# Kernel optimization log

Hardware: AMD Instinct MI355X
Metric: run time of the kernel (lower is better)

## Reference

```python
import jax, jax.numpy as jnp
import numpy as np

B, H, W, T, D = 8, 32, 32, 4, 768
BLK = 4  # super-block of base tokens used to generate the static partition


def _build_descs():
    """Deterministic partition: 4x4 blocks of the 32x32 grid, scale = block_idx % 3."""
    d0, d1, d2 = [], [], []
    for t in range(T):
        i = 0
        for by in range(0, H, BLK):
            for bx in range(0, W, BLK):
                s = i % 3
                i += 1
                if s == 0:  # 16 base (scale-0) tokens
                    for yy in range(by, by + BLK):
                        for xx in range(bx, bx + BLK):
                            d0.append((yy, xx, t))
                elif s == 1:  # four 2x2 (scale-1) tokens
                    for yy in range(by, by + BLK, 2):
                        for xx in range(bx, bx + BLK, 2):
                            d1.append((yy, xx, t))
                else:  # one 4x4 (scale-2) token
                    d2.append((by, bx, t))
    return (jnp.asarray(np.array(d0, dtype=np.int32)),
            jnp.asarray(np.array(d1, dtype=np.int32)),
            jnp.asarray(np.array(d2, dtype=np.int32)))


def setup_inputs() -> dict:
    key = jax.random.key(0)
    ks = jax.random.split(key, 8)
    base = jax.random.normal(ks[0], (B, H, W, T, D), dtype=jnp.float32)
    desc0, desc1, desc2 = _build_descs()  # [1408,3], [336,3], [84,3] of (y, x, t)
    ws = 0.05  # keep conv outputs O(1)
    w1 = jax.random.normal(ks[1], (D, D, 2, 2), jnp.float32) * ws
    b1 = jax.random.normal(ks[2], (D,), jnp.float32) * ws
    w2a = jax.random.normal(ks[3], (D, D, 2, 2), jnp.float32) * ws
    b2a = jax.random.normal(ks[4], (D,), jnp.float32) * ws
    w2b = jax.random.normal(ks[5], (D, D, 2, 2), jnp.float32) * ws
    b2b = jax.random.normal(ks[6], (D,), jnp.float32) * ws
    return {"base_patch_embeddings": base, "desc0": desc0, "desc1": desc1,
            "desc2": desc2, "w1": w1, "b1": b1, "w2a": w2a, "b2a": b2a,
            "w2b": w2b, "b2b": b2b}


def _gather_blocks(base, desc, S):
    """Gather [B, N, S, S, D] blocks at (y, x, t) descriptors."""
    off = jnp.arange(S)
    ys = desc[:, 0][:, None, None] + off[None, :, None]  # [N,S,1]
    xs = desc[:, 1][:, None, None] + off[None, None, :]  # [N,1,S]
    ts = desc[:, 2][:, None, None]                       # [N,1,1]
    return base[:, ys, xs, ts, :]                        # [B,N,S,S,D]


def _down(x, w, b):
    """One k=2, s=2 conv over grouped blocks: [B,N,S,S,D] -> [B,N,S/2,S/2,D]."""
    Bn, N, S, _, Dd = x.shape
    x = x.reshape(Bn, N, S // 2, 2, S // 2, 2, Dd)
    return jnp.einsum('bnhiwjc,dcij->bnhwd', x, w) + b


def reference(base_patch_embeddings, desc0, desc1, desc2, w1, b1, w2a, b2a, w2b, b2b):
    base = base_patch_embeddings
    # scale 0: direct gather of base tokens
    tok0 = base[:, desc0[:, 0], desc0[:, 1], desc0[:, 2], :]          # [B,N0,D]
    # scale 1: 2x2 blocks -> one conv
    blk1 = _gather_blocks(base, desc1, 2)                             # [B,N1,2,2,D]
    tok1 = _down(blk1, w1, b1)[:, :, 0, 0, :]                         # [B,N1,D]
    # scale 2: 4x4 blocks -> two convs
    blk2 = _gather_blocks(base, desc2, 4)                             # [B,N2,4,4,D]
    tok2 = _down(_down(blk2, w2a, b2a), w2b, b2b)[:, :, 0, 0, :]      # [B,N2,D]
    tokens = jnp.concatenate([tok0, tok1, tok2], axis=1)              # [B,1828,D]
    # positions: (y, x, size_in_base, timestep)
    def _pos(desc, size):
        n = desc.shape[0]
        return jnp.concatenate([desc[:, :2],
                                jnp.full((n, 1), size, jnp.int32),
                                desc[:, 2:3]], axis=1)
    positions = jnp.concatenate([_pos(desc0, 1), _pos(desc1, 2), _pos(desc2, 4)], axis=0)
    return tokens, positions
```

## Files before the change

### kernel.cpp

```cpp
#include <hip/hip_runtime.h>
#include <cstdint>
#include <cstddef>

#define BB    8
#define HH    32
#define WW    32
#define TT    4
#define DD    768
#define N0    1408
#define N1    336
#define N2    84
#define NTOK  1828
#define TOK_FLOATS (BB*NTOK*DD)
#define KDIM  3072
#define M1    (BB*N1)
#define M2A   (BB*N2*4)
#define M2B   (BB*N2)

typedef __attribute__((ext_vector_type(8))) short          short8v;
typedef __attribute__((ext_vector_type(8))) unsigned short us8;
typedef __attribute__((ext_vector_type(4))) float          f32x4;

__device__ __forceinline__ unsigned short f2bf(float f) {
    unsigned int u = __float_as_uint(f);
    u += 0x7fffu + ((u >> 16) & 1u);
    return (unsigned short)(u >> 16);
}

__device__ __forceinline__ void cp16(const unsigned short* g, unsigned short* l) {
    __builtin_amdgcn_global_load_lds(
        (const __attribute__((address_space(1))) unsigned int*)(const void*)g,
        (__attribute__((address_space(3))) unsigned int*)(void*)l,
        16, 0, 0);
}

#define GA_BLKS 8064
#define CW_BLKS 6912
#define G0_BLKS 2048
#define PREP_BLKS (GA_BLKS + CW_BLKS + G0_BLKS + 8)

__global__ __launch_bounds__(256) void prep_kernel(
    const float* __restrict__ base, const int* __restrict__ d0,
    const int* __restrict__ d1, const int* __restrict__ d2,
    const float* __restrict__ w1, const float* __restrict__ w2a,
    const float* __restrict__ w2b,
    unsigned short* __restrict__ A1, unsigned short* __restrict__ A2,
    unsigned short* __restrict__ W1, unsigned short* __restrict__ W2a,
    unsigned short* __restrict__ W2b,
    float* __restrict__ out, float* __restrict__ pos)
{
    const int blk = blockIdx.x, tid = threadIdx.x;
    if (blk < GA_BLKS) {
        int idx = blk * 256 + tid;
        int rm = idx / 384, o = idx - rm * 384;
        int s = (o & ~7) | ((o ^ rm) & 7);
        int p = s / 96, c0 = (s - p * 96) * 8;
        const float* rowp;
        unsigned short* dst;
        if (rm < M1) {
            int m = rm, b = m / N1, tok = m - b * N1;
            int y = d1[tok*3] + (p>>1), x = d1[tok*3+1] + (p&1), t = d1[tok*3+2];
            rowp = base + (size_t)(((b*HH + y)*WW + x)*TT + t) * DD;
            dst  = A1 + (size_t)m * KDIM + o * 8;
        } else {
            int m = rm - M1, b = m / (N2*4), r = m - b * (N2*4);
            int n = r >> 2, hw = r & 3, h = hw >> 1, w = hw & 1;
            int y = d2[n*3] + 2*h + (p>>1), x = d2[n*3+1] + 2*w + (p&1), t = d2[n*3+2];
            rowp = base + (size_t)(((b*HH + y)*WW + x)*TT + t) * DD;
            dst  = A2 + (size_t)m * KDIM + o * 8;
        }
        float4 v0 = *(const float4*)(rowp + c0);
        float4 v1 = *(const float4*)(rowp + c0 + 4);
        us8 r8;
        r8[0]=f2bf(v0.x); r8[1]=f2bf(v0.y); r8[2]=f2bf(v0.z); r8[3]=f2bf(v0.w);
        r8[4]=f2bf(v1.x); r8[5]=f2bf(v1.y); r8[6]=f2bf(v1.z); r8[7]=f2bf(v1.w);
        *(us8*)dst = r8;
    } else if (blk < GA_BLKS + CW_BLKS) {
        int r = blk - GA_BLKS;
        int wsel = r / 2304;
        int idx  = (r - wsel * 2304) * 256 + tid;
        const float* w        = wsel==0 ? w1 : (wsel==1 ? w2a : w2b);
        unsigned short* Wt    = wsel==0 ? W1 : (wsel==1 ? W2a : W2b);
        int d = idx / DD, c = idx - d * DD;
        float4 v = *(const float4*)(w + (size_t)d * KDIM + c * 4);
        int csw = (c & ~63) | ((((c>>3) ^ d) & 7) << 3) | (c & 7);
        unsigned short* o = Wt + (size_t)d * KDIM + csw;
        o[0*DD] = f2bf(v.x); o[1*DD] = f2bf(v.y); o[2*DD] = f2bf(v.z); o[3*DD] = f2bf(v.w);
    } else if (blk < GA_BLKS + CW_BLKS + G0_BLKS) {
        int bl = blk - GA_BLKS - CW_BLKS;
        const int total = BB * N0 * (DD/4);
        for (int idx = bl * 256 + tid; idx < total; idx += G0_BLKS * 256) {
            int d4 = idx % (DD/4);
            int nb = idx / (DD/4);
            int n  = nb % N0;
            int b  = nb / N0;
            int y = d0[n*3], x = d0[n*3+1], t = d0[n*3+2];
            const float4* src = (const float4*)(base + (size_t)(((b*HH + y)*WW + x)*TT + t) * DD) + d4;
            float4*       dst = (float4*)(out + ((size_t)b*NTOK + n) * DD) + d4;
            *dst = *src;
        }
    } else {
        int n = (blk - GA_BLKS - CW_BLKS - G0_BLKS) * 256 + tid;
        if (n >= NTOK) return;
        int y, x, t, s;
        if (n < N0)         { y = d0[n*3];         x = d0[n*3+1];         t = d0[n*3+2];       s = 1; }
        else if (n < N0+N1) { int m = n - N0;      y = d1[m*3]; x = d1[m*3+1]; t = d1[m*3+2];  s = 2; }
        else                { int m = n - N0 - N1; y = d2[m*3]; x = d2[m*3+1]; t = d2[m*3+2];  s = 4; }
        pos[n*4+0] = (float)y; pos[n*4+1] = (float)x; pos[n*4+2] = (float)s; pos[n*4+3] = (float)t;
    }
}

struct GCfg {
    const unsigned short* A;
    const unsigned short* Bw;
    const float*          bias;
    float*                outf;
    unsigned short*       outb;
    int                   M;
    int                   mode;
};

__global__ __launch_bounds__(256) void mfma_gemm_v3(
    GCfg c0, GCfg c1, int nper, int mblks, int swz)
{
    __shared__ unsigned short As[2][64 * 64];
    __shared__ unsigned short Bs[2][128 * 64];

    int wgid = blockIdx.x;
    if (swz) wgid = (wgid & 7) * (gridDim.x >> 3) + (wgid >> 3);
    GCfg cfg = c0;
    if (wgid >= nper) { cfg = c1; wgid -= nper; }
    const int nb = wgid / mblks, mb = wgid - nb * mblks;
    const int m0 = mb * 64, n0 = nb * 128;

    const int tid = threadIdx.x, lane = tid & 63;
    const int wv = tid >> 6, wr = wv >> 1, wc = wv & 1;
    const int lr = lane & 15, lq = lane >> 4, xr = lr & 7;

    const int aoct = tid & 7, trow = tid >> 3;
    int am0 = m0 + trow;      if (am0 >= cfg.M) am0 = cfg.M - 1;
    int am1 = m0 + 32 + trow; if (am1 >= cfg.M) am1 = cfg.M - 1;
    const unsigned short* ag0 = cfg.A + (size_t)am0 * KDIM + aoct * 8;
    const unsigned short* ag1 = cfg.A + (size_t)am1 * KDIM + aoct * 8;
    const unsigned short* bg0 = cfg.Bw + (size_t)(n0 +      trow) * KDIM + aoct * 8;
    const unsigned short* bg1 = cfg.Bw + (size_t)(n0 + 32 + trow) * KDIM + aoct * 8;
    const unsigned short* bg2 = cfg.Bw + (size_t)(n0 + 64 + trow) * KDIM + aoct * 8;
    const unsigned short* bg3 = cfg.Bw + (size_t)(n0 + 96 + trow) * KDIM + aoct * 8;

    const int wu = tid & 192;

    f32x4 acc[2][4];
    #pragma unroll
    for (int i = 0; i < 2; ++i)
        #pragma unroll
        for (int j = 0; j < 4; ++j)
            #pragma unroll
            for (int r = 0; r < 4; ++r) acc[i][j][r] = 0.f;

    auto STAGE = [&](int buf, int k0) {
        cp16(ag0 + k0, &As[buf][(0*256 + wu) * 8]);
        cp16(ag1 + k0, &As[buf][(1*256 + wu) * 8]);
        cp16(bg0 + k0, &Bs[buf][(0*256 + wu) * 8]);
        cp16(bg1 + k0, &Bs[buf][(1*256 + wu) * 8]);
        cp16(bg2 + k0, &Bs[buf][(2*256 + wu) * 8]);
        cp16(bg3 + k0, &Bs[buf][(3*256 + wu) * 8]);
    };

    STAGE(0, 0);
    constexpr int NIT = KDIM / 64;
    for (int it = 0; it < NIT; ++it) {
        const int cur = it & 1;
        if (it + 1 < NIT) {
            STAGE(cur ^ 1, (it + 1) * 64);
            asm volatile("s_waitcnt vmcnt(6)" ::: "memory");
        } else {
            asm volatile("s_waitcnt vmcnt(0)" ::: "memory");
        }
        __builtin_amdgcn_s_barrier();
        const unsigned short* Asb = As[cur];
        const unsigned short* Bsb = Bs[cur];
        #pragma unroll
        for (int ks = 0; ks < 2; ++ks) {
            short8v av[2], bv[4];
            #pragma unroll
            for (int fm = 0; fm < 2; ++fm) {
                int row = wr*32 + fm*16 + lr;
                av[fm] = *(const short8v*)&Asb[row*64 + ((ks*4 + lq) ^ xr) * 8];
            }
            #pragma unroll
            for (int fn = 0; fn < 4; ++fn) {
                int row = wc*64 + fn*16 + lr;
                bv[fn] = *(const short8v*)&Bsb[row*64 + ((ks*4 + lq) ^ xr) * 8];
            }
            #pragma unroll
            for (int fm = 0; fm < 2; ++fm)
                #pragma unroll
                for (int fn = 0; fn < 4; ++fn)
                    acc[fm][fn] = __builtin_amdgcn_mfma_f32_16x16x32_bf16(
                        av[fm], bv[fn], acc[fm][fn], 0, 0, 0);
        }
        __builtin_amdgcn_s_barrier();
    }

    const int mode = cfg.mode;
    #pragma unroll
    for (int fm = 0; fm < 2; ++fm) {
        #pragma unroll
        for (int fn = 0; fn < 4; ++fn) {
            int n = n0 + wc*64 + fn*16 + lr;
            float bs = cfg.bias[n];
            #pragma unroll
            for (int r = 0; r < 4; ++r) {
                int m = m0 + wr*32 + fm*16 + lq*4 + r;
                if (m >= cfg.M) continue;
                float v = acc[fm][fn][r] + bs;
                if (mode == 0) {
                    int b = m / N1, tok = m - b*N1;
                    cfg.outf[((size_t)b*NTOK + N0 + tok)*DD + n] = v;
                } else if (mode == 1) {
                    int nsw = (n & ~63) | ((((n>>3) ^ (m>>2)) & 7) << 3) | (n & 7);
                    cfg.outb[(size_t)m*DD + nsw] = f2bf(v);
                } else {
                    int b = m / N2, tk = m - b*N2;
                    cfg.outf[((size_t)b*NTOK + N0 + N1 + tk)*DD + n] = v;
                }
            }
        }
    }
}

extern "C" void kernel_launch(void* const* d_in, const int* in_sizes, int n_in,
                              void* d_out, int out_size, void* d_ws, size_t ws_size,
                              hipStream_t stream)
{
    const float* base  = (const float*)d_in[0];
    const int*   desc0 = (const int*)  d_in[1];
    const int*   desc1 = (const int*)  d_in[2];
    const int*   desc2 = (const int*)  d_in[3];
    const float* w1    = (const float*)d_in[4];
    const float* b1    = (const float*)d_in[5];
    const float* w2a   = (const float*)d_in[6];
    const float* b2a   = (const float*)d_in[7];
    const float* w2b   = (const float*)d_in[8];
    const float* b2b   = (const float*)d_in[9];

    float* out = (float*)d_out;
    float* pos = (float*)d_out + TOK_FLOATS;
    unsigned short* ws = (unsigned short*)d_ws;

    const size_t ABF = (size_t)M1 * KDIM;
    const size_t Y1  = (size_t)M2A * DD;
    const size_t WTB = (size_t)DD * KDIM;
    unsigned short* A1  = ws;
    unsigned short* A2  = A1  + ABF;
    unsigned short* y1b = A2  + ABF;
    unsigned short* W1  = y1b + Y1;
    unsigned short* W2a = W1  + WTB;
    unsigned short* W2b = W2a + WTB;

    prep_kernel<<<PREP_BLKS, 256, 0, stream>>>(
        base, desc0, desc1, desc2, w1, w2a, w2b,
        A1, A2, W1, W2a, W2b, out, pos);

    GCfg cA = { A1, W1,  b1,  out,     nullptr, M1,  0 };
    GCfg cB = { A2, W2a, b2a, nullptr, y1b,     M2A, 1 };
    mfma_gemm_v3<<<504, 256, 0, stream>>>(cA, cB, 252, 42, 1);

    GCfg cC = { y1b, W2b, b2b, out, nullptr, M2B, 2 };
    mfma_gemm_v3<<<66, 256, 0, stream>>>(cC, cC, 66, 11, 0);
}
```

Before: 296.4 us.

## Use 128x128 tiles with 32x32 MFMA, split-K final GEMM, and overlap gather copy

The GEMM tile grows from 64x128 to 128x128 and switches to the 32x32x16 bf16 MFMA, and workgroups are remapped per XCD. The last small GEMM is split along K into two halves that accumulate into a pre-zeroed output with atomics, so more workgroups run. The scale-0 token copy moves out of the prep kernel into extra blocks of the first GEMM launch so it overlaps the compute. The prep kernel's gather, weight-transpose and convert loops now handle wider chunks per thread. The costs are atomic traffic and fewer workgroups in the first GEMM from the larger tiles.

```diff
diff --git a/kernel.cpp b/kernel.cpp
--- a/kernel.cpp
+++ b/kernel.cpp
@@ -17,9 +17,10 @@
 #define M2A   (BB*N2*4)
 #define M2B   (BB*N2)
 
-typedef __attribute__((ext_vector_type(8))) short          short8v;
-typedef __attribute__((ext_vector_type(8))) unsigned short us8;
-typedef __attribute__((ext_vector_type(4))) float          f32x4;
+typedef __attribute__((ext_vector_type(8)))  short          short8v;
+typedef __attribute__((ext_vector_type(8)))  unsigned short us8;
+typedef __attribute__((ext_vector_type(4)))  unsigned short us4;
+typedef __attribute__((ext_vector_type(16))) float          f32x16;
 
 __device__ __forceinline__ unsigned short f2bf(float f) {
     unsigned int u = __float_as_uint(f);
@@ -34,10 +35,10 @@
         16, 0, 0);
 }
 
-#define GA_BLKS 8064
-#define CW_BLKS 6912
-#define G0_BLKS 2048
-#define PREP_BLKS (GA_BLKS + CW_BLKS + G0_BLKS + 8)
+#define GA_BLKS 1008
+#define CW_BLKS 1728
+#define Z_BLKS  504
+#define PREP_BLKS (GA_BLKS + CW_BLKS + Z_BLKS + 8)
 
 __global__ __launch_bounds__(256) void prep_kernel(
     const float* __restrict__ base, const int* __restrict__ d0,
@@ -52,55 +53,65 @@
     const int blk = blockIdx.x, tid = threadIdx.x;
     if (blk < GA_BLKS) {
         int idx = blk * 256 + tid;
-        int rm = idx / 384, o = idx - rm * 384;
-        int s = (o & ~7) | ((o ^ rm) & 7);
-        int p = s / 96, c0 = (s - p * 96) * 8;
+        int rm = idx / 48, sg = idx - rm * 48;
+        int key = rm & 7;
+        int p = sg / 12, cb = (sg - p * 12) * 64;
         const float* rowp;
         unsigned short* dst;
         if (rm < M1) {
             int m = rm, b = m / N1, tok = m - b * N1;
             int y = d1[tok*3] + (p>>1), x = d1[tok*3+1] + (p&1), t = d1[tok*3+2];
             rowp = base + (size_t)(((b*HH + y)*WW + x)*TT + t) * DD;
-            dst  = A1 + (size_t)m * KDIM + o * 8;
+            dst  = A1 + (size_t)m * KDIM + sg * 64;
         } else {
             int m = rm - M1, b = m / (N2*4), r = m - b * (N2*4);
             int n = r >> 2, hw = r & 3, h = hw >> 1, w = hw & 1;
             int y = d2[n*3] + 2*h + (p>>1), x = d2[n*3+1] + 2*w + (p&1), t = d2[n*3+2];
             rowp = base + (size_t)(((b*HH + y)*WW + x)*TT + t) * DD;
-            dst  = A2 + (size_t)m * KDIM + o * 8;
-        }
-        float4 v0 = *(const float4*)(rowp + c0);
-        float4 v1 = *(const float4*)(rowp + c0 + 4);
-        us8 r8;
-        r8[0]=f2bf(v0.x); r8[1]=f2bf(v0.y); r8[2]=f2bf(v0.z); r8[3]=f2bf(v0.w);
-        r8[4]=f2bf(v1.x); r8[5]=f2bf(v1.y); r8[6]=f2bf(v1.z); r8[7]=f2bf(v1.w);
-        *(us8*)dst = r8;
+            dst  = A2 + (size_t)m * KDIM + sg * 64;
+        }
+        float4 v[16];
+        #pragma unroll
+        for (int j = 0; j < 16; ++j) v[j] = *(const float4*)(rowp + cb + j*4);
+        #pragma unroll
+        for (int o = 0; o < 8; ++o) {
+            int s = o ^ key;
+            float4 lo = v[s*2], hi = v[s*2+1];
+            us8 r8;
+            r8[0]=f2bf(lo.x); r8[1]=f2bf(lo.y); r8[2]=f2bf(lo.z); r8[3]=f2bf(lo.w);
+            r8[4]=f2bf(hi.x); r8[5]=f2bf(hi.y); r8[6]=f2bf(hi.z); r8[7]=f2bf(hi.w);
+            *(us8*)(dst + o*8) = r8;
+        }
     } else if (blk < GA_BLKS + CW_BLKS) {
         int r = blk - GA_BLKS;
-        int wsel = r / 2304;
-        int idx  = (r - wsel * 2304) * 256 + tid;
-        const float* w        = wsel==0 ? w1 : (wsel==1 ? w2a : w2b);
-        unsigned short* Wt    = wsel==0 ? W1 : (wsel==1 ? W2a : W2b);
-        int d = idx / DD, c = idx - d * DD;
-        float4 v = *(const float4*)(w + (size_t)d * KDIM + c * 4);
-        int csw = (c & ~63) | ((((c>>3) ^ d) & 7) << 3) | (c & 7);
-        unsigned short* o = Wt + (size_t)d * KDIM + csw;
-        o[0*DD] = f2bf(v.x); o[1*DD] = f2bf(v.y); o[2*DD] = f2bf(v.z); o[3*DD] = f2bf(v.w);
-    } else if (blk < GA_BLKS + CW_BLKS + G0_BLKS) {
-        int bl = blk - GA_BLKS - CW_BLKS;
-        const int total = BB * N0 * (DD/4);
-        for (int idx = bl * 256 + tid; idx < total; idx += G0_BLKS * 256) {
-            int d4 = idx % (DD/4);
-            int nb = idx / (DD/4);
-            int n  = nb % N0;
-            int b  = nb / N0;
-            int y = d0[n*3], x = d0[n*3+1], t = d0[n*3+2];
-            const float4* src = (const float4*)(base + (size_t)(((b*HH + y)*WW + x)*TT + t) * DD) + d4;
-            float4*       dst = (float4*)(out + ((size_t)b*NTOK + n) * DD) + d4;
-            *dst = *src;
-        }
+        int wsel = r / 576;
+        int idx  = (r - wsel * 576) * 256 + tid;
+        const float* w     = wsel==0 ? w1 : (wsel==1 ? w2a : w2b);
+        unsigned short* Wt = wsel==0 ? W1 : (wsel==1 ? W2a : W2b);
+        int d = idx / 192, cg = idx - d * 192;
+        const float* src = w + (size_t)d * KDIM + cg * 16;
+        float4 v0 = ((const float4*)src)[0];
+        float4 v1 = ((const float4*)src)[1];
+        float4 v2 = ((const float4*)src)[2];
+        float4 v3 = ((const float4*)src)[3];
+        int csw = ((cg*4) & ~63) | ((((cg>>1) ^ d) & 7) << 3) | ((cg & 1) * 4);
+        unsigned short* ob = Wt + (size_t)d * KDIM + csw;
+        float pv[4][4] = {{v0.x,v1.x,v2.x,v3.x},{v0.y,v1.y,v2.y,v3.y},
+                          {v0.z,v1.z,v2.z,v3.z},{v0.w,v1.w,v2.w,v3.w}};
+        #pragma unroll
+        for (int p = 0; p < 4; ++p) {
+            us4 o4; o4[0]=f2bf(pv[p][0]); o4[1]=f2bf(pv[p][1]);
+                    o4[2]=f2bf(pv[p][2]); o4[3]=f2bf(pv[p][3]);
+            *(us4*)(ob + p*DD) = o4;
+        }
+    } else if (blk < GA_BLKS + CW_BLKS + Z_BLKS) {
+        int g = (blk - GA_BLKS - CW_BLKS) * 256 + tid;
+        int d4 = g % 192, r = g / 192;
+        int tk = r % N2, b = r / N2;
+        float4 z = {0.f, 0.f, 0.f, 0.f};
+        *(float4*)(out + ((size_t)b*NTOK + N0 + N1 + tk)*DD + d4*4) = z;
     } else {
-        int n = (blk - GA_BLKS - CW_BLKS - G0_BLKS) * 256 + tid;
+        int n = (blk - GA_BLKS - CW_BLKS - Z_BLKS) * 256 + tid;
         if (n >= NTOK) return;
         int y, x, t, s;
         if (n < N0)         { y = d0[n*3];         x = d0[n*3+1];         t = d0[n*3+2];       s = 1; }
@@ -118,61 +129,82 @@
     unsigned short*       outb;
     int                   M;
     int                   mode;
+    int                   kbeg;
+    int                   kend;
 };
 
-__global__ __launch_bounds__(256) void mfma_gemm_v3(
-    GCfg c0, GCfg c1, int nper, int mblks, int swz)
+__global__ __launch_bounds__(256) void mfma_gemm_v4(
+    GCfg c0, GCfg c1, int nper, int mblks, int ngemm,
+    const float* __restrict__ base, const int* __restrict__ d0,
+    float* __restrict__ out0)
 {
-    __shared__ unsigned short As[2][64 * 64];
+    if ((int)blockIdx.x >= ngemm) {
+        int g = ((int)blockIdx.x - ngemm) * 256 + threadIdx.x;
+        int r = g / 12, q = g - r * 12;
+        int b = r / N0, n = r - b * N0;
+        int y = d0[n*3], x = d0[n*3+1], t = d0[n*3+2];
+        const float4* src = (const float4*)(base + (size_t)(((b*HH + y)*WW + x)*TT + t) * DD + q*64);
+        float4*       dst = (float4*)(out0 + ((size_t)b*NTOK + n) * DD + q*64);
+        float4 v[16];
+        #pragma unroll
+        for (int j = 0; j < 16; ++j) v[j] = src[j];
+        #pragma unroll
+        for (int j = 0; j < 16; ++j) dst[j] = v[j];
+        return;
+    }
+
+    __shared__ unsigned short As[2][128 * 64];
     __shared__ unsigned short Bs[2][128 * 64];
 
-    int wgid = blockIdx.x;
-    if (swz) wgid = (wgid & 7) * (gridDim.x >> 3) + (wgid >> 3);
+    int wgid;
+    {
+        int nwg = ngemm, orig = blockIdx.x;
+        int q = nwg >> 3, r = nwg & 7;
+        int xcd = orig & 7, k = orig >> 3;
+        wgid = (xcd < r ? xcd * (q + 1) : r * (q + 1) + (xcd - r) * q) + k;
+    }
     GCfg cfg = c0;
     if (wgid >= nper) { cfg = c1; wgid -= nper; }
     const int nb = wgid / mblks, mb = wgid - nb * mblks;
-    const int m0 = mb * 64, n0 = nb * 128;
+    const int m0 = mb * 128, n0 = nb * 128;
 
     const int tid = threadIdx.x, lane = tid & 63;
     const int wv = tid >> 6, wr = wv >> 1, wc = wv & 1;
-    const int lr = lane & 15, lq = lane >> 4, xr = lr & 7;
-
-    const int aoct = tid & 7, trow = tid >> 3;
-    int am0 = m0 + trow;      if (am0 >= cfg.M) am0 = cfg.M - 1;
-    int am1 = m0 + 32 + trow; if (am1 >= cfg.M) am1 = cfg.M - 1;
-    const unsigned short* ag0 = cfg.A + (size_t)am0 * KDIM + aoct * 8;
-    const unsigned short* ag1 = cfg.A + (size_t)am1 * KDIM + aoct * 8;
-    const unsigned short* bg0 = cfg.Bw + (size_t)(n0 +      trow) * KDIM + aoct * 8;
-    const unsigned short* bg1 = cfg.Bw + (size_t)(n0 + 32 + trow) * KDIM + aoct * 8;
-    const unsigned short* bg2 = cfg.Bw + (size_t)(n0 + 64 + trow) * KDIM + aoct * 8;
-    const unsigned short* bg3 = cfg.Bw + (size_t)(n0 + 96 + trow) * KDIM + aoct * 8;
-
-    const int wu = tid & 192;
-
-    f32x4 acc[2][4];
+    const int l31 = lane & 31, l5 = lane >> 5;
+
+    const unsigned short* agp[4];
+    const unsigned short* bgp[4];
+    #pragma unroll
+    for (int j = 0; j < 4; ++j) {
+        int ar = m0 + j*32 + (tid >> 3); if (ar >= cfg.M) ar = cfg.M - 1;
+        agp[j] = cfg.A  + (size_t)ar * KDIM + cfg.kbeg + (tid & 7) * 8;
+        int br = n0 + j*32 + (tid >> 3);
+        bgp[j] = cfg.Bw + (size_t)br * KDIM + cfg.kbeg + (tid & 7) * 8;
+    }
+    const int wb = (tid >> 6) * 512;
+
+    f32x16 acc[2][2];
     #pragma unroll
     for (int i = 0; i < 2; ++i)
         #pragma unroll
-        for (int j = 0; j < 4; ++j)
-            #pragma unroll
-            for (int r = 0; r < 4; ++r) acc[i][j][r] = 0.f;
+        for (int j = 0; j < 2; ++j)
+            #pragma unroll
+            for (int r = 0; r < 16; ++r) acc[i][j][r] = 0.f;
 
     auto STAGE = [&](int buf, int k0) {
-        cp16(ag0 + k0, &As[buf][(0*256 + wu) * 8]);
-        cp16(ag1 + k0, &As[buf][(1*256 + wu) * 8]);
-        cp16(bg0 + k0, &Bs[buf][(0*256 + wu) * 8]);
-        cp16(bg1 + k0, &Bs[buf][(1*256 + wu) * 8]);
-        cp16(bg2 + k0, &Bs[buf][(2*256 + wu) * 8]);
-        cp16(bg3 + k0, &Bs[buf][(3*256 + wu) * 8]);
+        #pragma unroll
+        for (int j = 0; j < 4; ++j) cp16(agp[j] + k0, &As[buf][j*2048 + wb]);
+        #pragma unroll
+        for (int j = 0; j < 4; ++j) cp16(bgp[j] + k0, &Bs[buf][j*2048 + wb]);
     };
 
+    const int NIT = (cfg.kend - cfg.kbeg) >> 6;
     STAGE(0, 0);
-    constexpr int NIT = KDIM / 64;
     for (int it = 0; it < NIT; ++it) {
         const int cur = it & 1;
         if (it + 1 < NIT) {
             STAGE(cur ^ 1, (it + 1) * 64);
-            asm volatile("s_waitcnt vmcnt(6)" ::: "memory");
+            asm volatile("s_waitcnt vmcnt(8)" ::: "memory");
         } else {
             asm volatile("s_waitcnt vmcnt(0)" ::: "memory");
         }
@@ -180,23 +212,24 @@
         const unsigned short* Asb = As[cur];
         const unsigned short* Bsb = Bs[cur];
         #pragma unroll
-        for (int ks = 0; ks < 2; ++ks) {
-            short8v av[2], bv[4];
+        for (int ks = 0; ks < 4; ++ks) {
+            const int q = ks*2 + l5;
+            short8v av[2], bv[2];
             #pragma unroll
             for (int fm = 0; fm < 2; ++fm) {
-                int row = wr*32 + fm*16 + lr;
-                av[fm] = *(const short8v*)&Asb[row*64 + ((ks*4 + lq) ^ xr) * 8];
+                int R = wr*64 + fm*32 + l31;
+                av[fm] = *(const short8v*)&Asb[R*64 + ((q ^ (R&7)))*8];
             }
             #pragma unroll
-            for (int fn = 0; fn < 4; ++fn) {
-                int row = wc*64 + fn*16 + lr;
-                bv[fn] = *(const short8v*)&Bsb[row*64 + ((ks*4 + lq) ^ xr) * 8];
+            for (int fn = 0; fn < 2; ++fn) {
+                int R = wc*64 + fn*32 + l31;
+                bv[fn] = *(const short8v*)&Bsb[R*64 + ((q ^ (R&7)))*8];
             }
             #pragma unroll
             for (int fm = 0; fm < 2; ++fm)
                 #pragma unroll
-                for (int fn = 0; fn < 4; ++fn)
-                    acc[fm][fn] = __builtin_amdgcn_mfma_f32_16x16x32_bf16(
+                for (int fn = 0; fn < 2; ++fn)
+                    acc[fm][fn] = __builtin_amdgcn_mfma_f32_32x32x16_bf16(
                         av[fm], bv[fn], acc[fm][fn], 0, 0, 0);
         }
         __builtin_amdgcn_s_barrier();
@@ -206,23 +239,24 @@
     #pragma unroll
     for (int fm = 0; fm < 2; ++fm) {
         #pragma unroll
-        for (int fn = 0; fn < 4; ++fn) {
-            int n = n0 + wc*64 + fn*16 + lr;
+        for (int fn = 0; fn < 2; ++fn) {
+            int n = n0 + wc*64 + fn*32 + l31;
             float bs = cfg.bias[n];
             #pragma unroll
-            for (int r = 0; r < 4; ++r) {
-                int m = m0 + wr*32 + fm*16 + lq*4 + r;
+            for (int reg = 0; reg < 16; ++reg) {
+                int m = m0 + wr*64 + fm*32 + (reg&3) + 8*(reg>>2) + 4*l5;
                 if (m >= cfg.M) continue;
-                float v = acc[fm][fn][r] + bs;
+                float v = acc[fm][fn][reg];
                 if (mode == 0) {
                     int b = m / N1, tok = m - b*N1;
-                    cfg.outf[((size_t)b*NTOK + N0 + tok)*DD + n] = v;
+                    cfg.outf[((size_t)b*NTOK + N0 + tok)*DD + n] = v + bs;
                 } else if (mode == 1) {
                     int nsw = (n & ~63) | ((((n>>3) ^ (m>>2)) & 7) << 3) | (n & 7);
-                    cfg.outb[(size_t)m*DD + nsw] = f2bf(v);
+                    cfg.outb[(size_t)m*DD + nsw] = f2bf(v + bs);
                 } else {
                     int b = m / N2, tk = m - b*N2;
-                    cfg.outf[((size_t)b*NTOK + N0 + N1 + tk)*DD + n] = v;
+                    float add = v + (cfg.kbeg == 0 ? bs : 0.f);
+                    atomicAdd(&cfg.outf[((size_t)b*NTOK + N0 + N1 + tk)*DD + n], add);
                 }
             }
         }
@@ -262,10 +296,11 @@
         base, desc0, desc1, desc2, w1, w2a, w2b,
         A1, A2, W1, W2a, W2b, out, pos);
 
-    GCfg cA = { A1, W1,  b1,  out,     nullptr, M1,  0 };
-    GCfg cB = { A2, W2a, b2a, nullptr, y1b,     M2A, 1 };
-    mfma_gemm_v3<<<504, 256, 0, stream>>>(cA, cB, 252, 42, 1);
-
-    GCfg cC = { y1b, W2b, b2b, out, nullptr, M2B, 2 };
-    mfma_gemm_v3<<<66, 256, 0, stream>>>(cC, cC, 66, 11, 0);
-}
+    GCfg cA = { A1, W1,  b1,  out,     nullptr, M1,  0, 0, KDIM };
+    GCfg cB = { A2, W2a, b2a, nullptr, y1b,     M2A, 1, 0, KDIM };
+    mfma_gemm_v4<<<252 + 528, 256, 0, stream>>>(cA, cB, 126, 21, 252, base, desc0, out);
+
+    GCfg cC0 = { y1b, W2b, b2b, out, nullptr, M2B, 2, 0,        KDIM/2 };
+    GCfg cC1 = { y1b, W2b, b2b, out, nullptr, M2B, 2, KDIM/2,   KDIM   };
+    mfma_gemm_v4<<<72, 256, 0, stream>>>(cC0, cC1, 36, 6, 72, base, desc0, out);
+}
```

After: 345.4 us. +16.5%, slower.
